# Kernel tuning notes

Measured on AMD Instinct MI355X. Metric: run time of the kernel, lower is better.

## Reference

```python
import jax, jax.numpy as jnp
import numpy as np

N_NODES = 50000


def setup_inputs() -> dict:
    key = jax.random.key(0)
    ks = jax.random.split(key, 12)
    node_features = jax.random.normal(ks[0], (50000, 256), dtype=jnp.float32)
    hedge_features = jax.random.normal(ks[1], (25000, 128), dtype=jnp.float32)
    node_senders = jax.random.randint(ks[2], (800000,), 0, 50000, dtype=jnp.int32)
    node_receivers = jnp.sort(jax.random.randint(ks[3], (800000,), 0, 50000, dtype=jnp.int32))
    node_convolution = jax.random.uniform(ks[4], (800000, 1), dtype=jnp.float32)
    hedge2node_senders = jax.random.randint(ks[5], (400000,), 0, 25000, dtype=jnp.int32)
    hedge2node_receivers = jnp.sort(jax.random.randint(ks[6], (400000,), 0, 50000, dtype=jnp.int32))
    hedge2node_convolution = jax.random.uniform(ks[7], (400000, 1), dtype=jnp.float32)
    # Linear params (flax convention: y = x @ W + b, W is [in, out])
    W_msg = jax.random.normal(ks[8], (256, 256), dtype=jnp.float32) / np.sqrt(256.0)
    b_msg = jax.random.normal(ks[9], (256,), dtype=jnp.float32) * 0.01
    W_scale = jax.random.normal(ks[10], (128, 256), dtype=jnp.float32) / np.sqrt(128.0)
    b_scale = jax.random.normal(ks[11], (256,), dtype=jnp.float32) * 0.01
    return {
        "node_features": node_features,
        "hedge_features": hedge_features,
        "node_senders": node_senders,
        "node_receivers": node_receivers,
        "node_convolution": node_convolution,
        "hedge2node_senders": hedge2node_senders,
        "hedge2node_receivers": hedge2node_receivers,
        "hedge2node_convolution": hedge2node_convolution,
        "W_msg": W_msg,
        "b_msg": b_msg,
        "W_scale": W_scale,
        "b_scale": b_scale,
    }


def reference(node_features, hedge_features, node_senders, node_receivers,
              node_convolution, hedge2node_senders, hedge2node_receivers,
              hedge2node_convolution, W_msg, b_msg, W_scale, b_scale):
    # node -> node message pipeline: gather, Linear, per-edge scale, segment_sum
    sender_features = node_features[node_senders]                     # [E, Fin]
    messages = sender_features @ W_msg + b_msg                        # [E, Fout]
    scaled_messages = node_convolution * messages                     # [E, Fout]
    gathered_messages = jax.ops.segment_sum(
        scaled_messages, node_receivers, num_segments=N_NODES)        # [N, Fout]
    # hedge -> node scaling pipeline: gather, Linear, per-edge scale, segment_sum
    hedge_sender_features = hedge_features[hedge2node_senders]        # [E2, Fh]
    hedge_messages = hedge_sender_features @ W_scale + b_scale        # [E2, Fout]
    scaled_hedge_messages = hedge2node_convolution * hedge_messages   # [E2, Fout]
    gathered_scaling = jax.ops.segment_sum(
        scaled_hedge_messages, hedge2node_receivers, num_segments=N_NODES)  # [N, Fout]
    # Hadamard combine
    return gathered_scaling * gathered_messages
```

## Files before the change

kernel.cpp:

```cpp
#include <hip/hip_runtime.h>


typedef __attribute__((ext_vector_type(8))) short bf16x8;
typedef __attribute__((ext_vector_type(4))) float f32x4;

static __device__ __forceinline__ unsigned short f2bf(float f) {
  unsigned u = __float_as_uint(f);
  u += 0x7fff + ((u >> 16) & 1);
  return (unsigned short)(u >> 16);
}
static __device__ __forceinline__ float bf2f(unsigned short h) {
  return __uint_as_float((unsigned)h << 16);
}

__global__ __launch_bounds__(256) void prep_all(
    const float* __restrict__ X, const float* __restrict__ H,
    const int* __restrict__ rcv1, int E1,
    const int* __restrict__ rcv2, int E2, int N,
    const float* __restrict__ Wm, const float* __restrict__ Ws,
    unsigned short* __restrict__ Xb, unsigned short* __restrict__ Hb,
    int* __restrict__ ro1, int* __restrict__ ro2,
    unsigned short* __restrict__ WmT, unsigned short* __restrict__ WsT,
    int nX4, int nH4)
{
  __shared__ float t[32][33];
  const int tid = (int)threadIdx.x;
  int b = (int)blockIdx.x;

  const int bX  = (nX4 + 255) / 256;
  const int bH  = (nH4 + 255) / 256;
  const int bE1 = (E1 + 255) / 256;
  const int bE2 = (E2 + 255) / 256;

  if (b < bX) {
    const int i = b * 256 + tid;
    if (i < nX4) {
      const float4 v = reinterpret_cast<const float4*>(X)[i];
      reinterpret_cast<ushort4*>(Xb)[i] =
          make_ushort4(f2bf(v.x), f2bf(v.y), f2bf(v.z), f2bf(v.w));
    }
    return;
  }
  b -= bX;
  if (b < bH) {
    const int i = b * 256 + tid;
    if (i < nH4) {
      const float4 v = reinterpret_cast<const float4*>(H)[i];
      reinterpret_cast<ushort4*>(Hb)[i] =
          make_ushort4(f2bf(v.x), f2bf(v.y), f2bf(v.z), f2bf(v.w));
    }
    return;
  }
  b -= bH;
  if (b < bE1) {
    const int e = b * 256 + tid;
    if (e < E1) {
      const int c = rcv1[e];
      const int p = (e == 0) ? -1 : rcv1[e - 1];
      for (int n = p + 1; n <= c; ++n) ro1[n] = e;
      if (e == E1 - 1)
        for (int n = c + 1; n <= N; ++n) ro1[n] = E1;
    }
    return;
  }
  b -= bE1;
  if (b < bE2) {
    const int e = b * 256 + tid;
    if (e < E2) {
      const int c = rcv2[e];
      const int p = (e == 0) ? -1 : rcv2[e - 1];
      for (int n = p + 1; n <= c; ++n) ro2[n] = e;
      if (e == E2 - 1)
        for (int n = c + 1; n <= N; ++n) ro2[n] = E2;
    }
    return;
  }
  b -= bE2;
  {
    const float* W; unsigned short* WT; int K, Nn, tile;
    if (b < 64) { W = Wm; WT = WmT; K = 256; Nn = 256; tile = b; }
    else        { W = Ws; WT = WsT; K = 128; Nn = 256; tile = b - 64; }
    const int ntiles_n = Nn / 32;
    const int n0 = (tile % ntiles_n) * 32;
    const int k0 = (tile / ntiles_n) * 32;
    const int tx = tid & 31, ty = tid >> 5;
#pragma unroll
    for (int i = 0; i < 32; i += 8)
      t[ty + i][tx] = W[(size_t)(k0 + ty + i) * Nn + n0 + tx];
    __syncthreads();
#pragma unroll
    for (int i = 0; i < 32; i += 8)
      WT[(size_t)(n0 + ty + i) * K + k0 + tx] = f2bf(t[tx][ty + i]);
  }
}

__global__ __launch_bounds__(256) void scatter_node_seg(
    const unsigned short* __restrict__ X,
    const int* __restrict__ snd,
    const float* __restrict__ conv,
    const int* __restrict__ row_start,
    unsigned short* __restrict__ A,
    float* __restrict__ csum,
    int N)
{
  const int lane = threadIdx.x & 63;
  const int node = __builtin_amdgcn_readfirstlane(
      (int)blockIdx.x * 4 + ((int)threadIdx.x >> 6));
  if (node >= N) return;
  const int lo = row_start[node];
  const int hi = row_start[node + 1];

  const unsigned short* Xl = X + lane * 4;
  float4 acc = make_float4(0.f, 0.f, 0.f, 0.f);
  float cacc = 0.f;

  int e = lo;
  for (; e + 16 <= hi; e += 16) {
    int s[16]; float cv[16]; ushort4 x[16];
#pragma unroll
    for (int j = 0; j < 16; ++j) s[j] = snd[e + j];
#pragma unroll
    for (int j = 0; j < 16; ++j) cv[j] = conv[e + j];
#pragma unroll
    for (int j = 0; j < 16; ++j)
      x[j] = *reinterpret_cast<const ushort4*>(Xl + (size_t)s[j] * 256);
#pragma unroll
    for (int j = 0; j < 16; ++j) {
      acc.x = fmaf(cv[j], bf2f(x[j].x), acc.x);
      acc.y = fmaf(cv[j], bf2f(x[j].y), acc.y);
      acc.z = fmaf(cv[j], bf2f(x[j].z), acc.z);
      acc.w = fmaf(cv[j], bf2f(x[j].w), acc.w);
      cacc += cv[j];
    }
  }
  for (; e + 4 <= hi; e += 4) {
    int s[4]; float cv[4]; ushort4 x[4];
#pragma unroll
    for (int j = 0; j < 4; ++j) s[j] = snd[e + j];
#pragma unroll
    for (int j = 0; j < 4; ++j) cv[j] = conv[e + j];
#pragma unroll
    for (int j = 0; j < 4; ++j)
      x[j] = *reinterpret_cast<const ushort4*>(Xl + (size_t)s[j] * 256);
#pragma unroll
    for (int j = 0; j < 4; ++j) {
      acc.x = fmaf(cv[j], bf2f(x[j].x), acc.x);
      acc.y = fmaf(cv[j], bf2f(x[j].y), acc.y);
      acc.z = fmaf(cv[j], bf2f(x[j].z), acc.z);
      acc.w = fmaf(cv[j], bf2f(x[j].w), acc.w);
      cacc += cv[j];
    }
  }
  for (; e < hi; ++e) {
    const int s = snd[e];
    const float cv = conv[e];
    const ushort4 x = *reinterpret_cast<const ushort4*>(Xl + (size_t)s * 256);
    acc.x = fmaf(cv, bf2f(x.x), acc.x);
    acc.y = fmaf(cv, bf2f(x.y), acc.y);
    acc.z = fmaf(cv, bf2f(x.z), acc.z);
    acc.w = fmaf(cv, bf2f(x.w), acc.w);
    cacc += cv;
  }

  *reinterpret_cast<ushort4*>(A + (size_t)node * 256 + lane * 4) =
      make_ushort4(f2bf(acc.x), f2bf(acc.y), f2bf(acc.z), f2bf(acc.w));
  if (lane == 0) csum[node] = cacc;
}

__global__ __launch_bounds__(256) void scatter_hedge_seg(
    const unsigned short* __restrict__ X,
    const int* __restrict__ snd,
    const float* __restrict__ conv,
    const int* __restrict__ row_start,
    unsigned short* __restrict__ B,
    float* __restrict__ csum,
    int N)
{
  const int lane = threadIdx.x & 63;
  const int node = __builtin_amdgcn_readfirstlane(
      (int)blockIdx.x * 4 + ((int)threadIdx.x >> 6));
  if (node >= N) return;
  const int lo = row_start[node];
  const int hi = row_start[node + 1];

  const unsigned short* Xl = X + lane * 2;
  float2 acc = make_float2(0.f, 0.f);
  float cacc = 0.f;

  int e = lo;
  for (; e + 8 <= hi; e += 8) {
    int s[8]; float cv[8]; ushort2 x[8];
#pragma unroll
    for (int j = 0; j < 8; ++j) s[j] = snd[e + j];
#pragma unroll
    for (int j = 0; j < 8; ++j) cv[j] = conv[e + j];
#pragma unroll
    for (int j = 0; j < 8; ++j)
      x[j] = *reinterpret_cast<const ushort2*>(Xl + (size_t)s[j] * 128);
#pragma unroll
    for (int j = 0; j < 8; ++j) {
      acc.x = fmaf(cv[j], bf2f(x[j].x), acc.x);
      acc.y = fmaf(cv[j], bf2f(x[j].y), acc.y);
      cacc += cv[j];
    }
  }
  for (; e < hi; ++e) {
    const int s = snd[e];
    const float cv = conv[e];
    const ushort2 x = *reinterpret_cast<const ushort2*>(Xl + (size_t)s * 128);
    acc.x = fmaf(cv, bf2f(x.x), acc.x);
    acc.y = fmaf(cv, bf2f(x.y), acc.y);
    cacc += cv;
  }

  *reinterpret_cast<ushort2*>(B + (size_t)node * 128 + lane * 2) =
      make_ushort2(f2bf(acc.x), f2bf(acc.y));
  if (lane == 0) csum[node] = cacc;
}

__global__ __launch_bounds__(512) void gemm_combine_mfma(
    const unsigned short* __restrict__ A,
    const unsigned short* __restrict__ B,
    const float* __restrict__ c1,
    const float* __restrict__ c2,
    const unsigned short* __restrict__ WmT,
    const float* __restrict__ bm,
    const unsigned short* __restrict__ WsT,
    const float* __restrict__ bs,
    float* __restrict__ out,
    int M)
{
  __shared__ unsigned short lWm[64][264];
  __shared__ unsigned short lWs[64][136];

  const int tid  = (int)threadIdx.x;
  const int lane = tid & 63;
  const int wv   = tid >> 6;
  const int l15  = lane & 15;
  const int lg   = lane >> 4;
  const int m0      = blockIdx.x * 256;
  const int colBlk  = blockIdx.y * 64;

  for (int i = tid; i < 64 * 256 / 8; i += 512) {
    const int c = i >> 5, k8 = (i & 31) << 3;
    *reinterpret_cast<bf16x8*>(&lWm[c][k8]) =
        *reinterpret_cast<const bf16x8*>(WmT + (size_t)(colBlk + c) * 256 + k8);
  }
  for (int i = tid; i < 64 * 128 / 8; i += 512) {
    const int c = i >> 4, k8 = (i & 15) << 3;
    *reinterpret_cast<bf16x8*>(&lWs[c][k8]) =
        *reinterpret_cast<const bf16x8*>(WsT + (size_t)(colBlk + c) * 128 + k8);
  }
  __syncthreads();

  const int rowA = m0 + wv * 32 + l15;

  f32x4 accM[2][4];
  f32x4 accS[2][4];
#pragma unroll
  for (int ms = 0; ms < 2; ++ms)
#pragma unroll
    for (int n = 0; n < 4; ++n) {
      accM[ms][n] = (f32x4)0.f;
      accS[ms][n] = (f32x4)0.f;
    }

#pragma unroll
  for (int kc = 0; kc < 256; kc += 32) {
    const int ko = kc + lg * 8;
    const bf16x8 a0 = *reinterpret_cast<const bf16x8*>(A + (size_t)rowA * 256 + ko);
    const bf16x8 a1 = *reinterpret_cast<const bf16x8*>(A + (size_t)(rowA + 16) * 256 + ko);
#pragma unroll
    for (int n = 0; n < 4; ++n) {
      const bf16x8 w = *reinterpret_cast<const bf16x8*>(&lWm[l15 + n * 16][ko]);
      accM[0][n] = __builtin_amdgcn_mfma_f32_16x16x32_bf16(a0, w, accM[0][n], 0, 0, 0);
      accM[1][n] = __builtin_amdgcn_mfma_f32_16x16x32_bf16(a1, w, accM[1][n], 0, 0, 0);
    }
  }

#pragma unroll
  for (int kc = 0; kc < 128; kc += 32) {
    const int ko = kc + lg * 8;
    const bf16x8 b0 = *reinterpret_cast<const bf16x8*>(B + (size_t)rowA * 128 + ko);
    const bf16x8 b1 = *reinterpret_cast<const bf16x8*>(B + (size_t)(rowA + 16) * 128 + ko);
#pragma unroll
    for (int n = 0; n < 4; ++n) {
      const bf16x8 w = *reinterpret_cast<const bf16x8*>(&lWs[l15 + n * 16][ko]);
      accS[0][n] = __builtin_amdgcn_mfma_f32_16x16x32_bf16(b0, w, accS[0][n], 0, 0, 0);
      accS[1][n] = __builtin_amdgcn_mfma_f32_16x16x32_bf16(b1, w, accS[1][n], 0, 0, 0);
    }
  }

  float bmv[4], bsv[4];
#pragma unroll
  for (int n = 0; n < 4; ++n) {
    bmv[n] = bm[colBlk + n * 16 + l15];
    bsv[n] = bs[colBlk + n * 16 + l15];
  }
#pragma unroll
  for (int ms = 0; ms < 2; ++ms) {
    const int rbase = m0 + wv * 32 + ms * 16 + lg * 4;
#pragma unroll
    for (int r = 0; r < 4; ++r) {
      const int row = rbase + r;
      if (row < M) {
        const float k1 = c1[row];
        const float k2 = c2[row];
#pragma unroll
        for (int n = 0; n < 4; ++n) {
          const int col = colBlk + n * 16 + l15;
          const float mv = accM[ms][n][r] + k1 * bmv[n];
          const float sv = accS[ms][n][r] + k2 * bsv[n];
          out[(size_t)row * 256 + col] = mv * sv;
        }
      }
    }
  }
}

extern "C" void kernel_launch(void* const* d_in, const int* in_sizes, int n_in,
                              void* d_out, int out_size, void* d_ws, size_t ws_size,
                              hipStream_t stream) {
  const float* node_features  = (const float*)d_in[0];
  const float* hedge_features = (const float*)d_in[1];
  const int*   node_senders   = (const int*)d_in[2];
  const int*   node_receivers = (const int*)d_in[3];
  const float* node_conv      = (const float*)d_in[4];
  const int*   h2n_senders    = (const int*)d_in[5];
  const int*   h2n_receivers  = (const int*)d_in[6];
  const float* h2n_conv       = (const float*)d_in[7];
  const float* Wm             = (const float*)d_in[8];
  const float* bm             = (const float*)d_in[9];
  const float* Ws             = (const float*)d_in[10];
  const float* bs             = (const float*)d_in[11];
  float* out = (float*)d_out;

  const int M   = in_sizes[0] / 256;
  const int Nh  = in_sizes[1] / 128;
  const int E   = in_sizes[2];
  const int E2  = in_sizes[5];
  const int Mp  = ((M + 255) / 256) * 256;

  unsigned short* Ab  = (unsigned short*)d_ws;
  unsigned short* Bb  = Ab + (size_t)Mp * 256;
  unsigned short* Xb  = Bb + (size_t)Mp * 128;
  unsigned short* Hb  = Xb + (size_t)M * 256;
  unsigned short* WmT = Hb + (size_t)Nh * 128;
  unsigned short* WsT = WmT + 256 * 256;
  float* c1 = (float*)(WsT + 256 * 128);
  float* c2 = c1 + Mp;
  int*   ro1 = (int*)(c2 + Mp);
  int*   ro2 = ro1 + (M + 1);

  const int nX4 = M * 256 / 4, nH4 = Nh * 128 / 4;
  const int bX  = (nX4 + 255) / 256;
  const int bH  = (nH4 + 255) / 256;
  const int bE1 = (E + 255) / 256;
  const int bE2 = (E2 + 255) / 256;
  const int prep_blocks = bX + bH + bE1 + bE2 + 64 + 32;

  prep_all<<<prep_blocks, 256, 0, stream>>>(
      node_features, hedge_features,
      node_receivers, E, h2n_receivers, E2, M,
      Wm, Ws, Xb, Hb, ro1, ro2, WmT, WsT, nX4, nH4);

  scatter_node_seg<<<(M + 3) / 4, 256, 0, stream>>>(
      Xb, node_senders, node_conv, ro1, Ab, c1, M);
  scatter_hedge_seg<<<(M + 3) / 4, 256, 0, stream>>>(
      Hb, h2n_senders, h2n_conv, ro2, Bb, c2, M);

  gemm_combine_mfma<<<dim3(Mp / 256, 4), 512, 0, stream>>>(
      Ab, Bb, c1, c2, WmT, bm, WsT, bs, out, M);
}
```

Baseline: 136.8 us.

## Hold A/B fragments in registers across all column blocks; mask scatter tails

The GEMM-combine kernel now loads each wave's A and B row fragments into registers once and loops over the four 64-column weight blocks inside one block, reloading weights into LDS per block. Previously each of four grid columns re-read the same A/B rows from global memory. The change also removes the remainder loops in both scatter kernels by using a single 16-wide loop with clamped indices and zeroed conv weights, and widens the hedge unroll from 8 to 16. The costs are fewer blocks in the GEMM, higher register pressure, extra syncs for the weight reloads, and wasted gather loads on short segments.

Result: faster. 123.8 us (-9.5%).

```diff
diff --git a/kernel.cpp b/kernel.cpp
--- a/kernel.cpp
+++ b/kernel.cpp
@@ -114,13 +114,15 @@
   float4 acc = make_float4(0.f, 0.f, 0.f, 0.f);
   float cacc = 0.f;
 
-  int e = lo;
-  for (; e + 16 <= hi; e += 16) {
+  for (int e = lo; e < hi; e += 16) {
     int s[16]; float cv[16]; ushort4 x[16];
 #pragma unroll
-    for (int j = 0; j < 16; ++j) s[j] = snd[e + j];
-#pragma unroll
-    for (int j = 0; j < 16; ++j) cv[j] = conv[e + j];
+    for (int j = 0; j < 16; ++j) {
+      const int idx = e + j;
+      const int ic = idx < hi ? idx : hi - 1;
+      s[j]  = snd[ic];
+      cv[j] = idx < hi ? conv[ic] : 0.f;
+    }
 #pragma unroll
     for (int j = 0; j < 16; ++j)
       x[j] = *reinterpret_cast<const ushort4*>(Xl + (size_t)s[j] * 256);
@@ -132,34 +134,6 @@
       acc.w = fmaf(cv[j], bf2f(x[j].w), acc.w);
       cacc += cv[j];
     }
-  }
-  for (; e + 4 <= hi; e += 4) {
-    int s[4]; float cv[4]; ushort4 x[4];
-#pragma unroll
-    for (int j = 0; j < 4; ++j) s[j] = snd[e + j];
-#pragma unroll
-    for (int j = 0; j < 4; ++j) cv[j] = conv[e + j];
-#pragma unroll
-    for (int j = 0; j < 4; ++j)
-      x[j] = *reinterpret_cast<const ushort4*>(Xl + (size_t)s[j] * 256);
-#pragma unroll
-    for (int j = 0; j < 4; ++j) {
-      acc.x = fmaf(cv[j], bf2f(x[j].x), acc.x);
-      acc.y = fmaf(cv[j], bf2f(x[j].y), acc.y);
-      acc.z = fmaf(cv[j], bf2f(x[j].z), acc.z);
-      acc.w = fmaf(cv[j], bf2f(x[j].w), acc.w);
-      cacc += cv[j];
-    }
-  }
-  for (; e < hi; ++e) {
-    const int s = snd[e];
-    const float cv = conv[e];
-    const ushort4 x = *reinterpret_cast<const ushort4*>(Xl + (size_t)s * 256);
-    acc.x = fmaf(cv, bf2f(x.x), acc.x);
-    acc.y = fmaf(cv, bf2f(x.y), acc.y);
-    acc.z = fmaf(cv, bf2f(x.z), acc.z);
-    acc.w = fmaf(cv, bf2f(x.w), acc.w);
-    cacc += cv;
   }
 
   *reinterpret_cast<ushort4*>(A + (size_t)node * 256 + lane * 4) =
@@ -187,30 +161,24 @@
   float2 acc = make_float2(0.f, 0.f);
   float cacc = 0.f;
 
-  int e = lo;
-  for (; e + 8 <= hi; e += 8) {
-    int s[8]; float cv[8]; ushort2 x[8];
-#pragma unroll
-    for (int j = 0; j < 8; ++j) s[j] = snd[e + j];
-#pragma unroll
-    for (int j = 0; j < 8; ++j) cv[j] = conv[e + j];
-#pragma unroll
-    for (int j = 0; j < 8; ++j)
+  for (int e = lo; e < hi; e += 16) {
+    int s[16]; float cv[16]; ushort2 x[16];
+#pragma unroll
+    for (int j = 0; j < 16; ++j) {
+      const int idx = e + j;
+      const int ic = idx < hi ? idx : hi - 1;
+      s[j]  = snd[ic];
+      cv[j] = idx < hi ? conv[ic] : 0.f;
+    }
+#pragma unroll
+    for (int j = 0; j < 16; ++j)
       x[j] = *reinterpret_cast<const ushort2*>(Xl + (size_t)s[j] * 128);
 #pragma unroll
-    for (int j = 0; j < 8; ++j) {
+    for (int j = 0; j < 16; ++j) {
       acc.x = fmaf(cv[j], bf2f(x[j].x), acc.x);
       acc.y = fmaf(cv[j], bf2f(x[j].y), acc.y);
       cacc += cv[j];
     }
-  }
-  for (; e < hi; ++e) {
-    const int s = snd[e];
-    const float cv = conv[e];
-    const ushort2 x = *reinterpret_cast<const ushort2*>(Xl + (size_t)s * 128);
-    acc.x = fmaf(cv, bf2f(x.x), acc.x);
-    acc.y = fmaf(cv, bf2f(x.y), acc.y);
-    cacc += cv;
   }
 
   *reinterpret_cast<ushort2*>(B + (size_t)node * 128 + lane * 2) =
@@ -238,80 +206,106 @@
   const int wv   = tid >> 6;
   const int l15  = lane & 15;
   const int lg   = lane >> 4;
-  const int m0      = blockIdx.x * 256;
-  const int colBlk  = blockIdx.y * 64;
-
-  for (int i = tid; i < 64 * 256 / 8; i += 512) {
-    const int c = i >> 5, k8 = (i & 31) << 3;
-    *reinterpret_cast<bf16x8*>(&lWm[c][k8]) =
-        *reinterpret_cast<const bf16x8*>(WmT + (size_t)(colBlk + c) * 256 + k8);
-  }
-  for (int i = tid; i < 64 * 128 / 8; i += 512) {
-    const int c = i >> 4, k8 = (i & 15) << 3;
-    *reinterpret_cast<bf16x8*>(&lWs[c][k8]) =
-        *reinterpret_cast<const bf16x8*>(WsT + (size_t)(colBlk + c) * 128 + k8);
-  }
-  __syncthreads();
+  const int m0   = blockIdx.x * 256;
 
   const int rowA = m0 + wv * 32 + l15;
 
-  f32x4 accM[2][4];
-  f32x4 accS[2][4];
+  bf16x8 afrag[2][8];
+  bf16x8 bfrag[2][4];
+#pragma unroll
+  for (int k8 = 0; k8 < 8; ++k8) {
+    const int ko = k8 * 32 + lg * 8;
+    afrag[0][k8] = *reinterpret_cast<const bf16x8*>(A + (size_t)rowA * 256 + ko);
+    afrag[1][k8] = *reinterpret_cast<const bf16x8*>(A + (size_t)(rowA + 16) * 256 + ko);
+  }
+#pragma unroll
+  for (int k8 = 0; k8 < 4; ++k8) {
+    const int ko = k8 * 32 + lg * 8;
+    bfrag[0][k8] = *reinterpret_cast<const bf16x8*>(B + (size_t)rowA * 128 + ko);
+    bfrag[1][k8] = *reinterpret_cast<const bf16x8*>(B + (size_t)(rowA + 16) * 128 + ko);
+  }
+
+  float k1v[2][4], k2v[2][4];
 #pragma unroll
   for (int ms = 0; ms < 2; ++ms)
 #pragma unroll
+    for (int r = 0; r < 4; ++r) {
+      const int row = m0 + wv * 32 + ms * 16 + lg * 4 + r;
+      const bool v = row < M;
+      k1v[ms][r] = v ? c1[row] : 0.f;
+      k2v[ms][r] = v ? c2[row] : 0.f;
+    }
+
+  for (int cb = 0; cb < 4; ++cb) {
+    const int colBlk = cb * 64;
+    __syncthreads();
+#pragma unroll
+    for (int i = 0; i < 4; ++i) {
+      const int idx = tid + i * 512;
+      const int c = idx >> 5, k8b = (idx & 31) << 3;
+      *reinterpret_cast<bf16x8*>(&lWm[c][k8b]) =
+          *reinterpret_cast<const bf16x8*>(WmT + (size_t)(colBlk + c) * 256 + k8b);
+    }
+#pragma unroll
+    for (int i = 0; i < 2; ++i) {
+      const int idx = tid + i * 512;
+      const int c = idx >> 4, k8b = (idx & 15) << 3;
+      *reinterpret_cast<bf16x8*>(&lWs[c][k8b]) =
+          *reinterpret_cast<const bf16x8*>(WsT + (size_t)(colBlk + c) * 128 + k8b);
+    }
+    __syncthreads();
+
+    f32x4 accM[2][4];
+    f32x4 accS[2][4];
+#pragma unroll
+    for (int ms = 0; ms < 2; ++ms)
+#pragma unroll
+      for (int n = 0; n < 4; ++n) {
+        accM[ms][n] = (f32x4)0.f;
+        accS[ms][n] = (f32x4)0.f;
+      }
+
+#pragma unroll
+    for (int k8 = 0; k8 < 8; ++k8) {
+      const int ko = k8 * 32 + lg * 8;
+#pragma unroll
+      for (int n = 0; n < 4; ++n) {
+        const bf16x8 w = *reinterpret_cast<const bf16x8*>(&lWm[l15 + n * 16][ko]);
+        accM[0][n] = __builtin_amdgcn_mfma_f32_16x16x32_bf16(afrag[0][k8], w, accM[0][n], 0, 0, 0);
+        accM[1][n] = __builtin_amdgcn_mfma_f32_16x16x32_bf16(afrag[1][k8], w, accM[1][n], 0, 0, 0);
+      }
+    }
+#pragma unroll
+    for (int k8 = 0; k8 < 4; ++k8) {
+      const int ko = k8 * 32 + lg * 8;
+#pragma unroll
+      for (int n = 0; n < 4; ++n) {
+        const bf16x8 w = *reinterpret_cast<const bf16x8*>(&lWs[l15 + n * 16][ko]);
+        accS[0][n] = __builtin_amdgcn_mfma_f32_16x16x32_bf16(bfrag[0][k8], w, accS[0][n], 0, 0, 0);
+        accS[1][n] = __builtin_amdgcn_mfma_f32_16x16x32_bf16(bfrag[1][k8], w, accS[1][n], 0, 0, 0);
+      }
+    }
+
+    float bmv[4], bsv[4];
+#pragma unroll
     for (int n = 0; n < 4; ++n) {
-      accM[ms][n] = (f32x4)0.f;
-      accS[ms][n] = (f32x4)0.f;
-    }
-
-#pragma unroll
-  for (int kc = 0; kc < 256; kc += 32) {
-    const int ko = kc + lg * 8;
-    const bf16x8 a0 = *reinterpret_cast<const bf16x8*>(A + (size_t)rowA * 256 + ko);
-    const bf16x8 a1 = *reinterpret_cast<const bf16x8*>(A + (size_t)(rowA + 16) * 256 + ko);
-#pragma unroll
-    for (int n = 0; n < 4; ++n) {
-      const bf16x8 w = *reinterpret_cast<const bf16x8*>(&lWm[l15 + n * 16][ko]);
-      accM[0][n] = __builtin_amdgcn_mfma_f32_16x16x32_bf16(a0, w, accM[0][n], 0, 0, 0);
-      accM[1][n] = __builtin_amdgcn_mfma_f32_16x16x32_bf16(a1, w, accM[1][n], 0, 0, 0);
-    }
-  }
-
-#pragma unroll
-  for (int kc = 0; kc < 128; kc += 32) {
-    const int ko = kc + lg * 8;
-    const bf16x8 b0 = *reinterpret_cast<const bf16x8*>(B + (size_t)rowA * 128 + ko);
-    const bf16x8 b1 = *reinterpret_cast<const bf16x8*>(B + (size_t)(rowA + 16) * 128 + ko);
-#pragma unroll
-    for (int n = 0; n < 4; ++n) {
-      const bf16x8 w = *reinterpret_cast<const bf16x8*>(&lWs[l15 + n * 16][ko]);
-      accS[0][n] = __builtin_amdgcn_mfma_f32_16x16x32_bf16(b0, w, accS[0][n], 0, 0, 0);
-      accS[1][n] = __builtin_amdgcn_mfma_f32_16x16x32_bf16(b1, w, accS[1][n], 0, 0, 0);
-    }
-  }
-
-  float bmv[4], bsv[4];
-#pragma unroll
-  for (int n = 0; n < 4; ++n) {
-    bmv[n] = bm[colBlk + n * 16 + l15];
-    bsv[n] = bs[colBlk + n * 16 + l15];
-  }
-#pragma unroll
-  for (int ms = 0; ms < 2; ++ms) {
-    const int rbase = m0 + wv * 32 + ms * 16 + lg * 4;
-#pragma unroll
-    for (int r = 0; r < 4; ++r) {
-      const int row = rbase + r;
-      if (row < M) {
-        const float k1 = c1[row];
-        const float k2 = c2[row];
-#pragma unroll
-        for (int n = 0; n < 4; ++n) {
-          const int col = colBlk + n * 16 + l15;
-          const float mv = accM[ms][n][r] + k1 * bmv[n];
-          const float sv = accS[ms][n][r] + k2 * bsv[n];
-          out[(size_t)row * 256 + col] = mv * sv;
+      bmv[n] = bm[colBlk + n * 16 + l15];
+      bsv[n] = bs[colBlk + n * 16 + l15];
+    }
+#pragma unroll
+    for (int ms = 0; ms < 2; ++ms) {
+      const int rbase = m0 + wv * 32 + ms * 16 + lg * 4;
+#pragma unroll
+      for (int r = 0; r < 4; ++r) {
+        const int row = rbase + r;
+        if (row < M) {
+#pragma unroll
+          for (int n = 0; n < 4; ++n) {
+            const int col = colBlk + n * 16 + l15;
+            const float mv = accM[ms][n][r] + k1v[ms][r] * bmv[n];
+            const float sv = accS[ms][n][r] + k2v[ms][r] * bsv[n];
+            out[(size_t)row * 256 + col] = mv * sv;
+          }
         }
       }
     }
@@ -369,6 +363,6 @@
   scatter_hedge_seg<<<(M + 3) / 4, 256, 0, stream>>>(
       Hb, h2n_senders, h2n_conv, ro2, Bb, c2, M);
 
-  gemm_combine_mfma<<<dim3(Mp / 256, 4), 512, 0, stream>>>(
+  gemm_combine_mfma<<<Mp / 256, 512, 0, stream>>>(
       Ab, Bb, c1, c2, WmT, bm, WsT, bs, out, M);
 }
```
